# Performance work log

Hardware: AMD Instinct MI355X
Metric: run time of the kernel (lower is better)

Reference implementation:

```python
import jax, jax.numpy as jnp
import numpy as np

WS = 8       # window_size
DR = 2       # down_r
HD = 32      # head_dim
NHEAD = 6    # n_heads = input_dim // head_dim
C = 192      # input_dim = output_dim
SHIFT = WS // 2
DP = WS // DR            # pooled window side (4)
NQ = WS * WS             # 64 queries per window
NK = DP * DP             # 16 keys per window


def _rel_index():
    coords = np.array([[i, j] for i in range(WS) for j in range(WS)])        # (64,2)
    idx = coords[:, None, :] - coords[None, :, :] + WS - 1                    # (64,64,2)
    idx = idx[:, : (WS * WS) // DR // DR, :]                                  # (64,16,2) — faithful slice
    return idx


def _shift_mask(nh, nw):
    p, r, s = WS, DR, WS - SHIFT
    m = np.zeros((nh, nw, p, p, p // r, p // r), dtype=bool)
    m[-1, :, :s, :, s // r:, :] = True
    m[-1, :, s:, :, : s // r, :] = True
    m[:, -1, :, :s, :, s // r:] = True
    m[:, -1, :, s:, :, : s // r] = True
    return m.reshape(1, 1, nh * nw, p * p, (p // r) ** 2)  # (1,1,NW,64,16)


def setup_inputs() -> dict:
    key = jax.random.key(0)
    ks = jax.random.split(key, 10)
    d = {}
    d['x'] = jax.random.normal(ks[0], (4, 256, 256, C), dtype=jnp.float32)
    sc = C ** -0.5
    d['Wq'] = jax.random.normal(ks[1], (C, C), dtype=jnp.float32) * sc
    d['bq'] = jax.random.normal(ks[2], (C,), dtype=jnp.float32) * 0.01
    d['Wk'] = jax.random.normal(ks[3], (C, C), dtype=jnp.float32) * sc
    d['bk'] = jax.random.normal(ks[4], (C,), dtype=jnp.float32) * 0.01
    d['Wv'] = jax.random.normal(ks[5], (C, C), dtype=jnp.float32) * sc
    d['bv'] = jax.random.normal(ks[6], (C,), dtype=jnp.float32) * 0.01
    d['Wo'] = jax.random.normal(ks[7], (C, C), dtype=jnp.float32) * sc
    d['bo'] = jax.random.normal(ks[8], (C,), dtype=jnp.float32) * 0.01
    d['rel_table'] = jax.random.normal(ks[9], (NHEAD, 2 * WS - 1, 2 * WS - 1), dtype=jnp.float32) * 0.02
    return d


def reference(x, Wq, bq, Wk, bk, Wv, bv, Wo, bo, rel_table):
    b, H, W, c = x.shape
    nh, nw = H // WS, W // WS
    # cyclic shift (type != 'W')
    x = jnp.roll(x, (-SHIFT, -SHIFT), axis=(1, 2))
    # partition windows: b nh nw p p c
    xw = x.reshape(b, nh, WS, nw, WS, c).transpose(0, 1, 3, 2, 4, 5)
    # max-pool K/V source within each window (DRxDR)
    xd = xw.reshape(b, nh, nw, DP, DR, DP, DR, c).max(axis=(4, 6))
    xq = xw.reshape(b, nh * nw, NQ, c)
    xd = xd.reshape(b, nh * nw, NK, c)
    q = (xq @ Wq + bq).reshape(b, nh * nw, NQ, NHEAD, HD).transpose(3, 0, 1, 2, 4)
    k = (xd @ Wk + bk).reshape(b, nh * nw, NK, NHEAD, HD).transpose(3, 0, 1, 2, 4)
    v = (xd @ Wv + bv).reshape(b, nh * nw, NK, NHEAD, HD).transpose(3, 0, 1, 2, 4)
    scale = HD ** -0.5
    attn = jnp.einsum('hbwpc,hbwqc->hbwpq', q * scale, k)  # (H,B,NW,64,16)
    idx = _rel_index()
    bias = rel_table[:, idx[:, :, 0], idx[:, :, 1]]        # (H,64,16)
    attn = attn + bias[:, None, None]
    mask = jnp.asarray(_shift_mask(nh, nw))
    attn = jnp.where(mask, -jnp.inf, attn)
    probs = jax.nn.softmax(attn, axis=-1)
    out = jnp.einsum('hbwpq,hbwqc->hbwpc', probs, v)       # (H,B,NW,64,HD)
    out = out.transpose(1, 2, 3, 0, 4).reshape(b, nh * nw, NQ, NHEAD * HD)
    out = out @ Wo + bo
    out = out.reshape(b, nh, nw, WS, WS, c).transpose(0, 1, 3, 2, 4, 5).reshape(b, H, W, c)
    out = jnp.roll(out, (SHIFT, SHIFT), axis=(1, 2))
    return out
```

## Files before the change

kernel.cpp:

```cpp
#include <hip/hip_runtime.h>
#include <cstddef>


#define XSTR 196

typedef __attribute__((ext_vector_type(8))) short s16x8;
typedef __attribute__((ext_vector_type(4))) float f32x4;

__device__ __forceinline__ short f2bf(float f) {
    unsigned u = __float_as_uint(f);
    u = u + 0x7fffu + ((u >> 16) & 1u);
    return (short)(u >> 16);
}
__device__ __forceinline__ float bf2f(short h) {
    return __uint_as_float(((unsigned)(unsigned short)h) << 16);
}

#define MAT_S 73728
#define LO_S  36864
#define CT_S   3072
#define KC_S    512

__global__ __launch_bounds__(256)
void prep_w(const float* __restrict__ Wq, const float* __restrict__ Wk,
            const float* __restrict__ Wv, const float* __restrict__ Wo,
            unsigned short* __restrict__ ws)
{
    const int t = blockIdx.x * 256 + threadIdx.x;
    if (t >= 4 * 12 * 6 * 64) return;
    const int lane = t & 63;
    const int kc = (t >> 6) % 6;
    const int ct = (t / 384) % 12;
    const int m  = t / 4608;
    const float* W = (m == 0) ? Wq : (m == 1) ? Wk : (m == 2) ? Wv : Wo;
    const int n  = ct * 16 + (lane & 15);
    const int k0 = kc * 32 + ((lane >> 4) * 8);
    alignas(16) unsigned short hi[8];
    alignas(16) unsigned short lo[8];
    #pragma unroll
    for (int j = 0; j < 8; ++j) {
        const float f = W[(size_t)(k0 + j) * 192 + n];
        const short h = f2bf(f);
        hi[j] = (unsigned short)h;
        lo[j] = (unsigned short)f2bf(f - bf2f(h));
    }
    unsigned short* dst = ws + (size_t)m * MAT_S + ct * CT_S + kc * KC_S + lane * 8;
    *reinterpret_cast<uint4*>(dst)        = *reinterpret_cast<const uint4*>(hi);
    *reinterpret_cast<uint4*>(dst + LO_S) = *reinterpret_cast<const uint4*>(lo);
}

__global__ __launch_bounds__(256, 2)
void wmsa_fused(const float* __restrict__ x,
                const float* __restrict__ bq, const float* __restrict__ bk,
                const float* __restrict__ bv, const float* __restrict__ bo,
                const float* __restrict__ rt,
                const unsigned short* __restrict__ ws,
                float* __restrict__ out)
{
    __shared__ alignas(16) float s_xw[64 * XSTR];
    __shared__ alignas(16) float s_k [16 * 192];
    __shared__ alignas(16) float s_v [16 * 192];
    __shared__ alignas(16) float s_rt[6 * 225];

    const int tid  = threadIdx.x;
    const int widx = blockIdx.x;
    const int b  = widx >> 10;
    const int wh = (widx >> 5) & 31;
    const int wc = widx & 31;

    for (int idx = tid; idx < 64 * 48; idx += 256) {
        const int pix = idx / 48;
        const int c4  = idx - pix * 48;
        const int i = pix >> 3, j = pix & 7;
        const int row = (wh * 8 + i + 4) & 255;
        const int col = (wc * 8 + j + 4) & 255;
        const float4 v = *reinterpret_cast<const float4*>(
            x + ((size_t)((b * 256 + row) * 256 + col)) * 192 + c4 * 4);
        *reinterpret_cast<float4*>(&s_xw[pix * XSTR + c4 * 4]) = v;
    }
    for (int idx = tid; idx < 6 * 225; idx += 256) s_rt[idx] = rt[idx];
    __syncthreads();

    const int lane = tid & 63;
    const int w    = tid >> 6;
    const int wm   = w >> 1;
    const int wn   = w & 1;
    const int g    = lane >> 4;
    const int c15  = lane & 15;

    s16x8 kah[6], kal[6];
    {
        const int p0 = (c15 >> 2) * 16 + (c15 & 3) * 2;
        const float* r0 = &s_xw[(p0    ) * XSTR];
        const float* r1 = &s_xw[(p0 + 1) * XSTR];
        const float* r2 = &s_xw[(p0 + 8) * XSTR];
        const float* r3 = &s_xw[(p0 + 9) * XSTR];
        #pragma unroll
        for (int kc = 0; kc < 6; ++kc) {
            const int cb = kc * 32 + g * 8;
            #pragma unroll
            for (int j = 0; j < 8; ++j) {
                const float f = fmaxf(fmaxf(r0[cb + j], r1[cb + j]),
                                      fmaxf(r2[cb + j], r3[cb + j]));
                const short h = f2bf(f);
                kah[kc][j] = h;
                kal[kc][j] = f2bf(f - bf2f(h));
            }
        }
    }

    {
        const int isV = (w >> 1) & 1;
        const unsigned short* wsm = ws + (size_t)(1 + isV) * MAT_S;
        const float* bias = isV ? bv : bk;
        float* sdst = isV ? s_v : s_k;
        const int ct0 = (w & 1) * 6;
        #pragma unroll
        for (int ctl = 0; ctl < 6; ++ctl) {
            const int ct = ct0 + ctl;
            const unsigned short* bp = wsm + ct * CT_S + lane * 8;
            f32x4 a0 = {0.f,0.f,0.f,0.f}, a1 = a0, a2 = a0;
            #pragma unroll
            for (int kc = 0; kc < 6; ++kc) {
                const s16x8 bh = *reinterpret_cast<const s16x8*>(bp + kc * KC_S);
                const s16x8 bl = *reinterpret_cast<const s16x8*>(bp + kc * KC_S + LO_S);
                a0 = __builtin_amdgcn_mfma_f32_16x16x32_bf16(kah[kc], bh, a0, 0, 0, 0);
                a1 = __builtin_amdgcn_mfma_f32_16x16x32_bf16(kal[kc], bh, a1, 0, 0, 0);
                a2 = __builtin_amdgcn_mfma_f32_16x16x32_bf16(kah[kc], bl, a2, 0, 0, 0);
            }
            const float bb = bias[ct * 16 + c15];
            #pragma unroll
            for (int r = 0; r < 4; ++r)
                sdst[(g * 4 + r) * 192 + ct * 16 + c15] = a0[r] + a1[r] + a2[r] + bb;
        }
    }

    s16x8 qah[2][6], qal[2][6];
    #pragma unroll
    for (int mt = 0; mt < 2; ++mt) {
        const int rb = wm * 32 + mt * 16 + c15;
        #pragma unroll
        for (int kc = 0; kc < 6; ++kc) {
            const float* src = &s_xw[rb * XSTR + kc * 32 + g * 8];
            #pragma unroll
            for (int j = 0; j < 8; ++j) {
                const float f = src[j];
                const short h = f2bf(f);
                qah[mt][kc][j] = h;
                qal[mt][kc][j] = f2bf(f - bf2f(h));
            }
        }
    }
    __syncthreads();

    {
        #pragma unroll
        for (int ctl = 0; ctl < 6; ++ctl) {
            const int ct = wn * 6 + ctl;
            const unsigned short* bp = ws + ct * CT_S + lane * 8;
            const float bb = bq[ct * 16 + c15];
            #pragma unroll
            for (int mt = 0; mt < 2; ++mt) {
                f32x4 a0 = {0.f,0.f,0.f,0.f}, a1 = a0, a2 = a0;
                #pragma unroll
                for (int kc = 0; kc < 6; ++kc) {
                    const s16x8 bh = *reinterpret_cast<const s16x8*>(bp + kc * KC_S);
                    const s16x8 bl = *reinterpret_cast<const s16x8*>(bp + kc * KC_S + LO_S);
                    a0 = __builtin_amdgcn_mfma_f32_16x16x32_bf16(qah[mt][kc], bh, a0, 0, 0, 0);
                    a1 = __builtin_amdgcn_mfma_f32_16x16x32_bf16(qal[mt][kc], bh, a1, 0, 0, 0);
                    a2 = __builtin_amdgcn_mfma_f32_16x16x32_bf16(qah[mt][kc], bl, a2, 0, 0, 0);
                }
                #pragma unroll
                for (int r = 0; r < 4; ++r) {
                    const int p = wm * 32 + mt * 16 + g * 4 + r;
                    s_xw[p * XSTR + ct * 16 + c15] = a0[r] + a1[r] + a2[r] + bb;
                }
            }
        }
    }
    __syncthreads();

    {
        const float scale = 0.17677669529663687f;
        const bool lastrow = (wh == 31);
        const bool lastcol = (wc == 31);
        #pragma unroll
        for (int pass = 0; pass < 2; ++pass) {
            const int pair = tid + pass * 256;
            if (pair < 384) {
                const int h = pair >> 6;
                const int p = pair & 63;
                const int pi = p >> 3, pj = p & 7;

                float4 q4[8];
                #pragma unroll
                for (int c4 = 0; c4 < 8; ++c4)
                    q4[c4] = *reinterpret_cast<const float4*>(&s_xw[p * XSTR + h * 32 + c4 * 4]);

                float sc[16];
                #pragma unroll
                for (int q_ = 0; q_ < 16; ++q_) {
                    float s = 0.f;
                    #pragma unroll
                    for (int c4 = 0; c4 < 8; ++c4) {
                        const float4 k4 = *reinterpret_cast<const float4*>(
                            &s_k[q_ * 192 + h * 32 + c4 * 4]);
                        s = fmaf(q4[c4].x, k4.x, s);
                        s = fmaf(q4[c4].y, k4.y, s);
                        s = fmaf(q4[c4].z, k4.z, s);
                        s = fmaf(q4[c4].w, k4.w, s);
                    }
                    s *= scale;
                    const int qi = q_ >> 3, qj = q_ & 7;
                    s += s_rt[h * 225 + (pi - qi + 7) * 15 + (pj - qj + 7)];
                    const int ki = q_ >> 2, kj = q_ & 3;
                    const bool msk = (lastrow && ((pi < 4) != (ki < 2))) ||
                                     (lastcol && ((pj < 4) != (kj < 2)));
                    sc[q_] = msk ? -1e30f : s;
                }

                float m = sc[0];
                #pragma unroll
                for (int q_ = 1; q_ < 16; ++q_) m = fmaxf(m, sc[q_]);
                float sum = 0.f;
                #pragma unroll
                for (int q_ = 0; q_ < 16; ++q_) { sc[q_] = __expf(sc[q_] - m); sum += sc[q_]; }
                const float inv = 1.0f / sum;
                #pragma unroll
                for (int q_ = 0; q_ < 16; ++q_) sc[q_] *= inv;

                #pragma unroll
                for (int c4 = 0; c4 < 8; ++c4) {
                    float ox = 0.f, oy = 0.f, oz = 0.f, ow = 0.f;
                    #pragma unroll
                    for (int q_ = 0; q_ < 16; ++q_) {
                        const float4 v4 = *reinterpret_cast<const float4*>(
                            &s_v[q_ * 192 + h * 32 + c4 * 4]);
                        ox = fmaf(sc[q_], v4.x, ox);
                        oy = fmaf(sc[q_], v4.y, oy);
                        oz = fmaf(sc[q_], v4.z, oz);
                        ow = fmaf(sc[q_], v4.w, ow);
                    }
                    float4 o4; o4.x = ox; o4.y = oy; o4.z = oz; o4.w = ow;
                    *reinterpret_cast<float4*>(&s_xw[p * XSTR + h * 32 + c4 * 4]) = o4;
                }
            }
        }
    }
    __syncthreads();

    s16x8 oah[2][6], oal[2][6];
    #pragma unroll
    for (int mt = 0; mt < 2; ++mt) {
        const int rb = wm * 32 + mt * 16 + c15;
        #pragma unroll
        for (int kc = 0; kc < 6; ++kc) {
            const float* src = &s_xw[rb * XSTR + kc * 32 + g * 8];
            #pragma unroll
            for (int j = 0; j < 8; ++j) {
                const float f = src[j];
                const short h = f2bf(f);
                oah[mt][kc][j] = h;
                oal[mt][kc][j] = f2bf(f - bf2f(h));
            }
        }
    }

    {
        const unsigned short* wsm = ws + (size_t)3 * MAT_S;
        #pragma unroll
        for (int ctl = 0; ctl < 6; ++ctl) {
            const int ct = wn * 6 + ctl;
            const unsigned short* bp = wsm + ct * CT_S + lane * 8;
            const float bb = bo[ct * 16 + c15];
            #pragma unroll
            for (int mt = 0; mt < 2; ++mt) {
                f32x4 a0 = {0.f,0.f,0.f,0.f}, a1 = a0, a2 = a0;
                #pragma unroll
                for (int kc = 0; kc < 6; ++kc) {
                    const s16x8 bh = *reinterpret_cast<const s16x8*>(bp + kc * KC_S);
                    const s16x8 bl = *reinterpret_cast<const s16x8*>(bp + kc * KC_S + LO_S);
                    a0 = __builtin_amdgcn_mfma_f32_16x16x32_bf16(oah[mt][kc], bh, a0, 0, 0, 0);
                    a1 = __builtin_amdgcn_mfma_f32_16x16x32_bf16(oal[mt][kc], bh, a1, 0, 0, 0);
                    a2 = __builtin_amdgcn_mfma_f32_16x16x32_bf16(oah[mt][kc], bl, a2, 0, 0, 0);
                }
                #pragma unroll
                for (int r = 0; r < 4; ++r) {
                    const int p = wm * 32 + mt * 16 + g * 4 + r;
                    const int i = p >> 3, j = p & 7;
                    const int row = (wh * 8 + i + 4) & 255;
                    const int col = (wc * 8 + j + 4) & 255;
                    out[((size_t)((b * 256 + row) * 256 + col)) * 192 + ct * 16 + c15] =
                        a0[r] + a1[r] + a2[r] + bb;
                }
            }
        }
    }
}

extern "C" void kernel_launch(void* const* d_in, const int* in_sizes, int n_in,
                              void* d_out, int out_size, void* d_ws, size_t ws_size,
                              hipStream_t stream) {
    (void)in_sizes; (void)n_in; (void)out_size; (void)ws_size;
    const float* x  = (const float*)d_in[0];
    const float* Wq = (const float*)d_in[1];
    const float* bq = (const float*)d_in[2];
    const float* Wk = (const float*)d_in[3];
    const float* bk = (const float*)d_in[4];
    const float* Wv = (const float*)d_in[5];
    const float* bv = (const float*)d_in[6];
    const float* Wo = (const float*)d_in[7];
    const float* bo = (const float*)d_in[8];
    const float* rt = (const float*)d_in[9];
    float* out = (float*)d_out;
    unsigned short* ws = (unsigned short*)d_ws;

    hipLaunchKernelGGL(prep_w, dim3(72), dim3(256), 0, stream, Wq, Wk, Wv, Wo, ws);
    hipLaunchKernelGGL(wmsa_fused, dim3(4096), dim3(256), 0, stream,
                       x, bq, bk, bv, bo, rt, ws, out);
}
```

Baseline: 652.9 us.

## Swizzle shared-memory window tile, vectorize LDS reads, stage output for coalesced stores

Applies an XOR swizzle on float4 units of the shared window tile to reduce bank conflicts for the MFMA fragment loads and scalar writes. Fragment gathers now use float4 LDS reads instead of scalar loads. The output projection results are written back into shared memory and then stored to global memory with coalesced float4 writes instead of scattered scalar stores. This adds two extra barriers and a second pass over shared memory.

```diff
diff --git a/kernel.cpp b/kernel.cpp
--- a/kernel.cpp
+++ b/kernel.cpp
@@ -3,6 +3,7 @@
 
 
 #define XSTR 196
+#define KSTR 196
 
 typedef __attribute__((ext_vector_type(8))) short s16x8;
 typedef __attribute__((ext_vector_type(4))) float f32x4;
@@ -14,6 +15,9 @@
 }
 __device__ __forceinline__ float bf2f(short h) {
     return __uint_as_float(((unsigned)(unsigned short)h) << 16);
+}
+__device__ __forceinline__ int swzu(int row, int u) {
+    return u ^ ((row >> 1) & 7);
 }
 
 #define MAT_S 73728
@@ -58,8 +62,8 @@
                 float* __restrict__ out)
 {
     __shared__ alignas(16) float s_xw[64 * XSTR];
-    __shared__ alignas(16) float s_k [16 * 192];
-    __shared__ alignas(16) float s_v [16 * 192];
+    __shared__ alignas(16) float s_k [16 * KSTR];
+    __shared__ alignas(16) float s_v [16 * KSTR];
     __shared__ alignas(16) float s_rt[6 * 225];
 
     const int tid  = threadIdx.x;
@@ -76,7 +80,7 @@
         const int col = (wc * 8 + j + 4) & 255;
         const float4 v = *reinterpret_cast<const float4*>(
             x + ((size_t)((b * 256 + row) * 256 + col)) * 192 + c4 * 4);
-        *reinterpret_cast<float4*>(&s_xw[pix * XSTR + c4 * 4]) = v;
+        reinterpret_cast<float4*>(&s_xw[pix * XSTR])[swzu(pix, c4)] = v;
     }
     for (int idx = tid; idx < 6 * 225; idx += 256) s_rt[idx] = rt[idx];
     __syncthreads();
@@ -91,20 +95,36 @@
     s16x8 kah[6], kal[6];
     {
         const int p0 = (c15 >> 2) * 16 + (c15 & 3) * 2;
-        const float* r0 = &s_xw[(p0    ) * XSTR];
-        const float* r1 = &s_xw[(p0 + 1) * XSTR];
-        const float* r2 = &s_xw[(p0 + 8) * XSTR];
-        const float* r3 = &s_xw[(p0 + 9) * XSTR];
         #pragma unroll
         for (int kc = 0; kc < 6; ++kc) {
-            const int cb = kc * 32 + g * 8;
+            const int u0 = kc * 8 + g * 2;
+            float4 m0, m1;
+            {
+                const float4 a0 = reinterpret_cast<const float4*>(&s_xw[(p0    ) * XSTR])[swzu(p0    , u0)];
+                const float4 b0 = reinterpret_cast<const float4*>(&s_xw[(p0 + 1) * XSTR])[swzu(p0 + 1, u0)];
+                const float4 c0 = reinterpret_cast<const float4*>(&s_xw[(p0 + 8) * XSTR])[swzu(p0 + 8, u0)];
+                const float4 d0 = reinterpret_cast<const float4*>(&s_xw[(p0 + 9) * XSTR])[swzu(p0 + 9, u0)];
+                m0.x = fmaxf(fmaxf(a0.x, b0.x), fmaxf(c0.x, d0.x));
+                m0.y = fmaxf(fmaxf(a0.y, b0.y), fmaxf(c0.y, d0.y));
+                m0.z = fmaxf(fmaxf(a0.z, b0.z), fmaxf(c0.z, d0.z));
+                m0.w = fmaxf(fmaxf(a0.w, b0.w), fmaxf(c0.w, d0.w));
+            }
+            {
+                const float4 a1 = reinterpret_cast<const float4*>(&s_xw[(p0    ) * XSTR])[swzu(p0    , u0 + 1)];
+                const float4 b1 = reinterpret_cast<const float4*>(&s_xw[(p0 + 1) * XSTR])[swzu(p0 + 1, u0 + 1)];
+                const float4 c1 = reinterpret_cast<const float4*>(&s_xw[(p0 + 8) * XSTR])[swzu(p0 + 8, u0 + 1)];
+                const float4 d1 = reinterpret_cast<const float4*>(&s_xw[(p0 + 9) * XSTR])[swzu(p0 + 9, u0 + 1)];
+                m1.x = fmaxf(fmaxf(a1.x, b1.x), fmaxf(c1.x, d1.x));
+                m1.y = fmaxf(fmaxf(a1.y, b1.y), fmaxf(c1.y, d1.y));
+                m1.z = fmaxf(fmaxf(a1.z, b1.z), fmaxf(c1.z, d1.z));
+                m1.w = fmaxf(fmaxf(a1.w, b1.w), fmaxf(c1.w, d1.w));
+            }
+            const float mv[8] = {m0.x, m0.y, m0.z, m0.w, m1.x, m1.y, m1.z, m1.w};
             #pragma unroll
             for (int j = 0; j < 8; ++j) {
-                const float f = fmaxf(fmaxf(r0[cb + j], r1[cb + j]),
-                                      fmaxf(r2[cb + j], r3[cb + j]));
-                const short h = f2bf(f);
+                const short h = f2bf(mv[j]);
                 kah[kc][j] = h;
-                kal[kc][j] = f2bf(f - bf2f(h));
+                kal[kc][j] = f2bf(mv[j] - bf2f(h));
             }
         }
     }
@@ -131,7 +151,7 @@
             const float bb = bias[ct * 16 + c15];
             #pragma unroll
             for (int r = 0; r < 4; ++r)
-                sdst[(g * 4 + r) * 192 + ct * 16 + c15] = a0[r] + a1[r] + a2[r] + bb;
+                sdst[(g * 4 + r) * KSTR + ct * 16 + c15] = a0[r] + a1[r] + a2[r] + bb;
         }
     }
 
@@ -141,13 +161,15 @@
         const int rb = wm * 32 + mt * 16 + c15;
         #pragma unroll
         for (int kc = 0; kc < 6; ++kc) {
-            const float* src = &s_xw[rb * XSTR + kc * 32 + g * 8];
+            const int u0 = kc * 8 + g * 2;
+            const float4 f0 = reinterpret_cast<const float4*>(&s_xw[rb * XSTR])[swzu(rb, u0)];
+            const float4 f1 = reinterpret_cast<const float4*>(&s_xw[rb * XSTR])[swzu(rb, u0 + 1)];
+            const float fv[8] = {f0.x, f0.y, f0.z, f0.w, f1.x, f1.y, f1.z, f1.w};
             #pragma unroll
             for (int j = 0; j < 8; ++j) {
-                const float f = src[j];
-                const short h = f2bf(f);
+                const short h = f2bf(fv[j]);
                 qah[mt][kc][j] = h;
-                qal[mt][kc][j] = f2bf(f - bf2f(h));
+                qal[mt][kc][j] = f2bf(fv[j] - bf2f(h));
             }
         }
     }
@@ -159,6 +181,8 @@
             const int ct = wn * 6 + ctl;
             const unsigned short* bp = ws + ct * CT_S + lane * 8;
             const float bb = bq[ct * 16 + c15];
+            const int uq = ct * 4 + (c15 >> 2);
+            const int eq = c15 & 3;
             #pragma unroll
             for (int mt = 0; mt < 2; ++mt) {
                 f32x4 a0 = {0.f,0.f,0.f,0.f}, a1 = a0, a2 = a0;
@@ -173,7 +197,7 @@
                 #pragma unroll
                 for (int r = 0; r < 4; ++r) {
                     const int p = wm * 32 + mt * 16 + g * 4 + r;
-                    s_xw[p * XSTR + ct * 16 + c15] = a0[r] + a1[r] + a2[r] + bb;
+                    s_xw[p * XSTR + swzu(p, uq) * 4 + eq] = a0[r] + a1[r] + a2[r] + bb;
                 }
             }
         }
@@ -195,7 +219,7 @@
                 float4 q4[8];
                 #pragma unroll
                 for (int c4 = 0; c4 < 8; ++c4)
-                    q4[c4] = *reinterpret_cast<const float4*>(&s_xw[p * XSTR + h * 32 + c4 * 4]);
+                    q4[c4] = reinterpret_cast<const float4*>(&s_xw[p * XSTR])[swzu(p, h * 8 + c4)];
 
                 float sc[16];
                 #pragma unroll
@@ -204,7 +228,7 @@
                     #pragma unroll
                     for (int c4 = 0; c4 < 8; ++c4) {
                         const float4 k4 = *reinterpret_cast<const float4*>(
-                            &s_k[q_ * 192 + h * 32 + c4 * 4]);
+                            &s_k[q_ * KSTR + h * 32 + c4 * 4]);
                         s = fmaf(q4[c4].x, k4.x, s);
                         s = fmaf(q4[c4].y, k4.y, s);
                         s = fmaf(q4[c4].z, k4.z, s);
@@ -235,14 +259,14 @@
                     #pragma unroll
                     for (int q_ = 0; q_ < 16; ++q_) {
                         const float4 v4 = *reinterpret_cast<const float4*>(
-                            &s_v[q_ * 192 + h * 32 + c4 * 4]);
+                            &s_v[q_ * KSTR + h * 32 + c4 * 4]);
                         ox = fmaf(sc[q_], v4.x, ox);
                         oy = fmaf(sc[q_], v4.y, oy);
                         oz = fmaf(sc[q_], v4.z, oz);
                         ow = fmaf(sc[q_], v4.w, ow);
                     }
                     float4 o4; o4.x = ox; o4.y = oy; o4.z = oz; o4.w = ow;
-                    *reinterpret_cast<float4*>(&s_xw[p * XSTR + h * 32 + c4 * 4]) = o4;
+                    reinterpret_cast<float4*>(&s_xw[p * XSTR])[swzu(p, h * 8 + c4)] = o4;
                 }
             }
         }
@@ -255,16 +279,19 @@
         const int rb = wm * 32 + mt * 16 + c15;
         #pragma unroll
         for (int kc = 0; kc < 6; ++kc) {
-            const float* src = &s_xw[rb * XSTR + kc * 32 + g * 8];
+            const int u0 = kc * 8 + g * 2;
+            const float4 f0 = reinterpret_cast<const float4*>(&s_xw[rb * XSTR])[swzu(rb, u0)];
+            const float4 f1 = reinterpret_cast<const float4*>(&s_xw[rb * XSTR])[swzu(rb, u0 + 1)];
+            const float fv[8] = {f0.x, f0.y, f0.z, f0.w, f1.x, f1.y, f1.z, f1.w};
             #pragma unroll
             for (int j = 0; j < 8; ++j) {
-                const float f = src[j];
-                const short h = f2bf(f);
+                const short h = f2bf(fv[j]);
                 oah[mt][kc][j] = h;
-                oal[mt][kc][j] = f2bf(f - bf2f(h));
-            }
-        }
-    }
+                oal[mt][kc][j] = f2bf(fv[j] - bf2f(h));
+            }
+        }
+    }
+    __syncthreads();
 
     {
         const unsigned short* wsm = ws + (size_t)3 * MAT_S;
@@ -273,6 +300,8 @@
             const int ct = wn * 6 + ctl;
             const unsigned short* bp = wsm + ct * CT_S + lane * 8;
             const float bb = bo[ct * 16 + c15];
+            const int uo = ct * 4 + (c15 >> 2);
+            const int eo = c15 & 3;
             #pragma unroll
             for (int mt = 0; mt < 2; ++mt) {
                 f32x4 a0 = {0.f,0.f,0.f,0.f}, a1 = a0, a2 = a0;
@@ -287,14 +316,24 @@
                 #pragma unroll
                 for (int r = 0; r < 4; ++r) {
                     const int p = wm * 32 + mt * 16 + g * 4 + r;
-                    const int i = p >> 3, j = p & 7;
-                    const int row = (wh * 8 + i + 4) & 255;
-                    const int col = (wc * 8 + j + 4) & 255;
-                    out[((size_t)((b * 256 + row) * 256 + col)) * 192 + ct * 16 + c15] =
-                        a0[r] + a1[r] + a2[r] + bb;
-                }
-            }
-        }
+                    s_xw[p * XSTR + swzu(p, uo) * 4 + eo] = a0[r] + a1[r] + a2[r] + bb;
+                }
+            }
+        }
+    }
+    __syncthreads();
+
+    #pragma unroll
+    for (int it = 0; it < 12; ++it) {
+        const int idx = tid + it * 256;
+        const int pix = idx / 48;
+        const int c4  = idx - pix * 48;
+        const float4 v = reinterpret_cast<const float4*>(&s_xw[pix * XSTR])[swzu(pix, c4)];
+        const int i = pix >> 3, j = pix & 7;
+        const int row = (wh * 8 + i + 4) & 255;
+        const int col = (wc * 8 + j + 4) & 255;
+        *reinterpret_cast<float4*>(
+            out + ((size_t)((b * 256 + row) * 256 + col)) * 192 + c4 * 4) = v;
     }
 }
 
```

After: 679.1 us. 1.04x slower.
